# Performance work log

Measured on AMD Instinct MI355X. Metric: run time of the kernel, lower is better.

## Reference

```python
import math
import jax, jax.numpy as jnp
import numpy as np

N, T, F, H = 30000, 4, 128, 8  # num_node, num_type, num_fea, num_head
D = F // H


def setup_inputs() -> dict:
    key = jax.random.key(0)
    k0, k1, k2, k3, k4 = jax.random.split(key, 5)
    feature = jax.random.normal(k0, (N, F), dtype=jnp.float32)
    edge_fea = jax.random.normal(k1, (N, T, F), dtype=jnp.float32)
    node_multi_mask = jax.random.randint(k2, (N,), 0, T)
    # Xavier-uniform-like scale for [*, F, F] projection tables
    xav = math.sqrt(6.0 / (F + F))
    node_proj = jax.random.uniform(k3, (T, F, F), minval=-xav, maxval=xav, dtype=jnp.float32)
    edge_proj = jax.random.uniform(k4, (T * T, F, F), minval=-xav, maxval=xav, dtype=jnp.float32)
    return {
        "feature": feature,
        "edge_fea": edge_fea,
        "node_multi_mask": node_multi_mask,
        "node_proj": node_proj,
        "edge_proj": edge_proj,
    }


def reference(feature, edge_fea, node_multi_mask, node_proj, edge_proj):
    # Type-indexed projections. Instead of gathering per-node [F,F] matrices
    # (which would materialize N*F*F), compute projections for all T source
    # types in one batched einsum, then select each node's type with a gather.
    # node: out[n] = node_proj[mask[n]] @ feature[n]
    node_all = jnp.einsum('tgf,nf->ntg', node_proj, feature)           # [N,T,F]
    node_p = jnp.take_along_axis(node_all, node_multi_mask[:, None, None], axis=1)[:, 0]  # [N,F]
    # edge: out[n,j] = edge_proj[mask[n]*T + j] @ edge_fea[n,j]
    edge_proj_r = edge_proj.reshape(T, T, F, F)                         # [src_type, j, F, F]
    edge_all = jnp.einsum('stgf,ntf->nstg', edge_proj_r, edge_fea)      # [N,T_src,T,F]
    edge_p = jnp.take_along_axis(edge_all, node_multi_mask[:, None, None, None], axis=1)[:, 0]  # [N,T,F]

    # multi-head attention weights
    node_multi_in = node_p.reshape(N, 1, H, D).transpose(0, 2, 1, 3) / math.sqrt(D)  # [N,H,1,D]
    edge_multi_in = edge_p.reshape(N, T, H, D).transpose(0, 2, 3, 1)                  # [N,H,D,T]
    scores = jnp.matmul(node_multi_in, edge_multi_in)                                 # [N,H,1,T]
    # NOTE: original uses nn.Softmax(dim=1) -> softmax over the HEAD axis
    all_r_weight = jax.nn.softmax(scores, axis=1).transpose(0, 3, 1, 2)               # [N,T,H,1]
    return all_r_weight
```

## Files before the change

### kernel.cpp

```cpp
#include <hip/hip_runtime.h>
#include <hip/hip_bf16.h>

#define N_NODES 30000
#define T_TYPES 4
#define F_DIM   128
#define H_HEADS 8

typedef __bf16 bf16x8 __attribute__((ext_vector_type(8)));
typedef __bf16 bf16x4 __attribute__((ext_vector_type(4)));
typedef float  floatx4 __attribute__((ext_vector_type(4)));

#define WS_REORDER 64
#define WS_NPB     480256
#define WS_EPB     611328

template <int CTRL>
static __device__ __forceinline__ float dpp_add(float x) {
    int xi = __builtin_bit_cast(int, x);
    int yi = __builtin_amdgcn_update_dpp(xi, xi, CTRL, 0xF, 0xF, true);
    return x + __builtin_bit_cast(float, yi);
}
static __device__ __forceinline__ float sum16(float x) {
    x = dpp_add<0xB1>(x);
    x = dpp_add<0x4E>(x);
    x = dpp_add<0x141>(x);
    x = dpp_add<0x140>(x);
    return x;
}

__global__ __launch_bounds__(256) void prep_kernel(
    const float* __restrict__ node_proj, const float* __restrict__ edge_proj,
    __bf16* __restrict__ npb, __bf16* __restrict__ epb, int* __restrict__ counts)
{
    int i = blockIdx.x * 256 + threadIdx.x;
    if (i < 4) counts[i] = 0;
    int base = i * 4;
    float4 v;
    __bf16* dst;
    if (base < T_TYPES * F_DIM * F_DIM) {
        v = ((const float4*)node_proj)[i];
        dst = npb + base;
    } else {
        int off = base - T_TYPES * F_DIM * F_DIM;
        v = ((const float4*)edge_proj)[off >> 2];
        dst = epb + off;
    }
    bf16x4 w = { (__bf16)v.x, (__bf16)v.y, (__bf16)v.z, (__bf16)v.w };
    *(bf16x4*)dst = w;
}

__global__ __launch_bounds__(256) void bucket_kernel(
    const int* __restrict__ mask, int* __restrict__ counts, int* __restrict__ reorder)
{
    int n = blockIdx.x * 256 + threadIdx.x;
    int lane = threadIdx.x & 63;
    int t = (n < N_NODES) ? mask[n] : -1;
    #pragma unroll
    for (int tt = 0; tt < T_TYPES; ++tt) {
        unsigned long long b = __ballot(t == tt);
        if (b == 0ull) continue;
        int cnt = __popcll(b);
        int leader = __ffsll((unsigned long long)b) - 1;
        int base = 0;
        if (lane == leader) base = atomicAdd(&counts[tt], cnt);
        base = __shfl(base, leader);
        if (t == tt) {
            int prefix = __popcll(b & ((1ull << lane) - 1ull));
            reorder[tt * N_NODES + base + prefix] = n;
        }
    }
}

__global__ __launch_bounds__(512) void main_kernel(
    const float* __restrict__ feature, const float* __restrict__ edge_fea,
    const int* __restrict__ counts, const int* __restrict__ reorder,
    const __bf16* __restrict__ npb, const __bf16* __restrict__ epb,
    float* __restrict__ out)
{
    const int b = blockIdx.x;
    const int t = b & 3;
    const int start = (b >> 2) * 32;
    const int Nt = counts[t];
    if (start >= Nt) return;
    const int valid = min(32, Nt - start);

    __shared__ __bf16 Afeat[32][136];
    __shared__ __bf16 Aedge[4][32][136];
    __shared__ float  sc[32][4][H_HEADS];
    __shared__ int    nidx[32];

    const int tid = threadIdx.x;
    if (tid < 32) {
        int s = (tid < valid) ? tid : (valid - 1);
        nidx[tid] = reorder[t * N_NODES + start + s];
    }
    __syncthreads();

    const int colv = tid & 31;
    const int rowg = tid >> 5;
    #pragma unroll
    for (int it = 0; it < 2; ++it) {
        int row = it * 16 + rowg;
        float4 v = ((const float4*)(feature + (long)nidx[row] * F_DIM))[colv];
        bf16x4 w = { (__bf16)v.x, (__bf16)v.y, (__bf16)v.z, (__bf16)v.w };
        *(bf16x4*)(&Afeat[row][0] + colv * 4) = w;
    }
    #pragma unroll
    for (int it = 0; it < 8; ++it) {
        int row = it * 16 + rowg;
        int j = row >> 5, r = row & 31;
        float4 v = ((const float4*)(edge_fea + ((long)nidx[r] * 4 + j) * F_DIM))[colv];
        bf16x4 w = { (__bf16)v.x, (__bf16)v.y, (__bf16)v.z, (__bf16)v.w };
        *(bf16x4*)(&Aedge[j][r][0] + colv * 4) = w;
    }
    __syncthreads();

    const int lane = tid & 63;
    const int wave = tid >> 6;
    const int ml   = lane & 15;
    const int quad = lane >> 4;
    const int g0   = wave * 16;

    floatx4 accN[2] = {};
    {
        const __bf16* a0 = &Afeat[ml][quad * 8];
        const __bf16* a1 = &Afeat[16 + ml][quad * 8];
        const __bf16* b0 = npb + t * (F_DIM * F_DIM) + (g0 + ml) * F_DIM + quad * 8;
        #pragma unroll
        for (int k0 = 0; k0 < 128; k0 += 32) {
            bf16x8 A0 = *(const bf16x8*)(a0 + k0);
            bf16x8 A1 = *(const bf16x8*)(a1 + k0);
            bf16x8 B0 = *(const bf16x8*)(b0 + k0);
            accN[0] = __builtin_amdgcn_mfma_f32_16x16x32_bf16(A0, B0, accN[0], 0, 0, 0);
            accN[1] = __builtin_amdgcn_mfma_f32_16x16x32_bf16(A1, B0, accN[1], 0, 0, 0);
        }
    }

    #pragma unroll
    for (int j = 0; j < 4; ++j) {
        floatx4 accE[2] = {};
        const __bf16* a0 = &Aedge[j][ml][quad * 8];
        const __bf16* a1 = &Aedge[j][16 + ml][quad * 8];
        const __bf16* b0 = epb + (t * 4 + j) * (F_DIM * F_DIM) + (g0 + ml) * F_DIM + quad * 8;
        #pragma unroll
        for (int k0 = 0; k0 < 128; k0 += 32) {
            bf16x8 A0 = *(const bf16x8*)(a0 + k0);
            bf16x8 A1 = *(const bf16x8*)(a1 + k0);
            bf16x8 B0 = *(const bf16x8*)(b0 + k0);
            accE[0] = __builtin_amdgcn_mfma_f32_16x16x32_bf16(A0, B0, accE[0], 0, 0, 0);
            accE[1] = __builtin_amdgcn_mfma_f32_16x16x32_bf16(A1, B0, accE[1], 0, 0, 0);
        }
        #pragma unroll
        for (int mt = 0; mt < 2; ++mt) {
            floatx4 p = accN[mt] * accE[mt];
            p.x = sum16(p.x);
            p.y = sum16(p.y);
            p.z = sum16(p.z);
            p.w = sum16(p.w);
            if (ml == 0) {
                int mb = mt * 16 + quad * 4;
                sc[mb + 0][j][wave] = p.x * 0.25f;
                sc[mb + 1][j][wave] = p.y * 0.25f;
                sc[mb + 2][j][wave] = p.z * 0.25f;
                sc[mb + 3][j][wave] = p.w * 0.25f;
            }
        }
    }
    __syncthreads();

    if (tid < 128) {
        int node = tid >> 2, j = tid & 3;
        if (node < valid) {
            float v[8], m = -1e30f;
            #pragma unroll
            for (int h = 0; h < 8; ++h) { v[h] = sc[node][j][h]; m = fmaxf(m, v[h]); }
            float s = 0.f;
            #pragma unroll
            for (int h = 0; h < 8; ++h) { v[h] = __expf(v[h] - m); s += v[h]; }
            float r = 1.0f / s;
            float* o = out + (long)nidx[node] * (T_TYPES * H_HEADS) + j * H_HEADS;
            float4 o0 = { v[0] * r, v[1] * r, v[2] * r, v[3] * r };
            float4 o1 = { v[4] * r, v[5] * r, v[6] * r, v[7] * r };
            ((float4*)o)[0] = o0;
            ((float4*)o)[1] = o1;
        }
    }
}

extern "C" void kernel_launch(void* const* d_in, const int* in_sizes, int n_in,
                              void* d_out, int out_size, void* d_ws, size_t ws_size,
                              hipStream_t stream) {
    const float* feature   = (const float*)d_in[0];
    const float* edge_fea  = (const float*)d_in[1];
    const int*   mask      = (const int*)d_in[2];
    const float* node_proj = (const float*)d_in[3];
    const float* edge_proj = (const float*)d_in[4];
    float* out = (float*)d_out;

    char* ws = (char*)d_ws;
    int*    counts  = (int*)ws;
    int*    reorder = (int*)(ws + WS_REORDER);
    __bf16* npb     = (__bf16*)(ws + WS_NPB);
    __bf16* epb     = (__bf16*)(ws + WS_EPB);

    prep_kernel<<<320, 256, 0, stream>>>(node_proj, edge_proj, npb, epb, counts);
    bucket_kernel<<<(N_NODES + 255) / 256, 256, 0, stream>>>(mask, counts, reorder);
    int nblk = ((N_NODES + 31) / 32) * T_TYPES;
    main_kernel<<<nblk, 512, 0, stream>>>(feature, edge_fea, counts, reorder, npb, epb, out);
}
```

Baseline: 145.3 us.

## Replace type bucketing with dense all-type projection and masked score selection

Removes the bucket/reorder kernel and the per-type block grid. Each block now processes 32 consecutive nodes and computes projections for all four source types, keeping only the scores matching each node's type. This trades 4x more MFMA work for contiguous loads, one fewer launch, no atomics and no early-exiting blocks. Launch bounds also request higher occupancy.

New measurement: 196.0 us. 34.9% more time.

```diff
diff --git a/kernel.cpp b/kernel.cpp
--- a/kernel.cpp
+++ b/kernel.cpp
@@ -10,9 +10,8 @@
 typedef __bf16 bf16x4 __attribute__((ext_vector_type(4)));
 typedef float  floatx4 __attribute__((ext_vector_type(4)));
 
-#define WS_REORDER 64
-#define WS_NPB     480256
-#define WS_EPB     611328
+#define WS_NPB 0
+#define WS_EPB 131072
 
 template <int CTRL>
 static __device__ __forceinline__ float dpp_add(float x) {
@@ -30,10 +29,9 @@
 
 __global__ __launch_bounds__(256) void prep_kernel(
     const float* __restrict__ node_proj, const float* __restrict__ edge_proj,
-    __bf16* __restrict__ npb, __bf16* __restrict__ epb, int* __restrict__ counts)
+    __bf16* __restrict__ npb, __bf16* __restrict__ epb)
 {
     int i = blockIdx.x * 256 + threadIdx.x;
-    if (i < 4) counts[i] = 0;
     int base = i * 4;
     float4 v;
     __bf16* dst;
@@ -49,69 +47,42 @@
     *(bf16x4*)dst = w;
 }
 
-__global__ __launch_bounds__(256) void bucket_kernel(
-    const int* __restrict__ mask, int* __restrict__ counts, int* __restrict__ reorder)
-{
-    int n = blockIdx.x * 256 + threadIdx.x;
-    int lane = threadIdx.x & 63;
-    int t = (n < N_NODES) ? mask[n] : -1;
-    #pragma unroll
-    for (int tt = 0; tt < T_TYPES; ++tt) {
-        unsigned long long b = __ballot(t == tt);
-        if (b == 0ull) continue;
-        int cnt = __popcll(b);
-        int leader = __ffsll((unsigned long long)b) - 1;
-        int base = 0;
-        if (lane == leader) base = atomicAdd(&counts[tt], cnt);
-        base = __shfl(base, leader);
-        if (t == tt) {
-            int prefix = __popcll(b & ((1ull << lane) - 1ull));
-            reorder[tt * N_NODES + base + prefix] = n;
-        }
-    }
-}
-
-__global__ __launch_bounds__(512) void main_kernel(
+__global__ __launch_bounds__(512, 6) void main_kernel(
     const float* __restrict__ feature, const float* __restrict__ edge_fea,
-    const int* __restrict__ counts, const int* __restrict__ reorder,
+    const int* __restrict__ mask,
     const __bf16* __restrict__ npb, const __bf16* __restrict__ epb,
     float* __restrict__ out)
 {
     const int b = blockIdx.x;
-    const int t = b & 3;
-    const int start = (b >> 2) * 32;
-    const int Nt = counts[t];
-    if (start >= Nt) return;
-    const int valid = min(32, Nt - start);
+    const int n0 = b * 32;
+    const int valid = min(32, N_NODES - n0);
 
     __shared__ __bf16 Afeat[32][136];
     __shared__ __bf16 Aedge[4][32][136];
     __shared__ float  sc[32][4][H_HEADS];
-    __shared__ int    nidx[32];
+    __shared__ int    tys[32];
 
     const int tid = threadIdx.x;
-    if (tid < 32) {
-        int s = (tid < valid) ? tid : (valid - 1);
-        nidx[tid] = reorder[t * N_NODES + start + s];
-    }
-    __syncthreads();
+    if (tid < 32) tys[tid] = (tid < valid) ? mask[n0 + tid] : -1;
 
     const int colv = tid & 31;
     const int rowg = tid >> 5;
     #pragma unroll
     for (int it = 0; it < 2; ++it) {
         int row = it * 16 + rowg;
-        float4 v = ((const float4*)(feature + (long)nidx[row] * F_DIM))[colv];
+        int r = min(row, valid - 1);
+        float4 v = ((const float4*)(feature + (long)(n0 + r) * F_DIM))[colv];
         bf16x4 w = { (__bf16)v.x, (__bf16)v.y, (__bf16)v.z, (__bf16)v.w };
         *(bf16x4*)(&Afeat[row][0] + colv * 4) = w;
     }
     #pragma unroll
     for (int it = 0; it < 8; ++it) {
         int row = it * 16 + rowg;
-        int j = row >> 5, r = row & 31;
-        float4 v = ((const float4*)(edge_fea + ((long)nidx[r] * 4 + j) * F_DIM))[colv];
+        int j = row >> 5, r0 = row & 31;
+        int r = min(r0, valid - 1);
+        float4 v = ((const float4*)(edge_fea + ((long)(n0 + r) * 4 + j) * F_DIM))[colv];
         bf16x4 w = { (__bf16)v.x, (__bf16)v.y, (__bf16)v.z, (__bf16)v.w };
-        *(bf16x4*)(&Aedge[j][r][0] + colv * 4) = w;
+        *(bf16x4*)(&Aedge[j][r0][0] + colv * 4) = w;
     }
     __syncthreads();
 
@@ -121,48 +92,58 @@
     const int quad = lane >> 4;
     const int g0   = wave * 16;
 
-    floatx4 accN[2] = {};
-    {
-        const __bf16* a0 = &Afeat[ml][quad * 8];
-        const __bf16* a1 = &Afeat[16 + ml][quad * 8];
-        const __bf16* b0 = npb + t * (F_DIM * F_DIM) + (g0 + ml) * F_DIM + quad * 8;
-        #pragma unroll
-        for (int k0 = 0; k0 < 128; k0 += 32) {
-            bf16x8 A0 = *(const bf16x8*)(a0 + k0);
-            bf16x8 A1 = *(const bf16x8*)(a1 + k0);
-            bf16x8 B0 = *(const bf16x8*)(b0 + k0);
-            accN[0] = __builtin_amdgcn_mfma_f32_16x16x32_bf16(A0, B0, accN[0], 0, 0, 0);
-            accN[1] = __builtin_amdgcn_mfma_f32_16x16x32_bf16(A1, B0, accN[1], 0, 0, 0);
-        }
-    }
-
     #pragma unroll
-    for (int j = 0; j < 4; ++j) {
-        floatx4 accE[2] = {};
-        const __bf16* a0 = &Aedge[j][ml][quad * 8];
-        const __bf16* a1 = &Aedge[j][16 + ml][quad * 8];
-        const __bf16* b0 = epb + (t * 4 + j) * (F_DIM * F_DIM) + (g0 + ml) * F_DIM + quad * 8;
-        #pragma unroll
-        for (int k0 = 0; k0 < 128; k0 += 32) {
-            bf16x8 A0 = *(const bf16x8*)(a0 + k0);
-            bf16x8 A1 = *(const bf16x8*)(a1 + k0);
-            bf16x8 B0 = *(const bf16x8*)(b0 + k0);
-            accE[0] = __builtin_amdgcn_mfma_f32_16x16x32_bf16(A0, B0, accE[0], 0, 0, 0);
-            accE[1] = __builtin_amdgcn_mfma_f32_16x16x32_bf16(A1, B0, accE[1], 0, 0, 0);
+    for (int tg = 0; tg < 2; ++tg) {
+        floatx4 accN[2][2] = {};
+        {
+            const __bf16* a0 = &Afeat[ml][quad * 8];
+            const __bf16* a1 = &Afeat[16 + ml][quad * 8];
+            const __bf16* bp = npb + (tg * 2) * (F_DIM * F_DIM) + (g0 + ml) * F_DIM + quad * 8;
+            #pragma unroll
+            for (int k0 = 0; k0 < 128; k0 += 32) {
+                bf16x8 A0 = *(const bf16x8*)(a0 + k0);
+                bf16x8 A1 = *(const bf16x8*)(a1 + k0);
+                bf16x8 B0 = *(const bf16x8*)(bp + k0);
+                bf16x8 B1 = *(const bf16x8*)(bp + F_DIM * F_DIM + k0);
+                accN[0][0] = __builtin_amdgcn_mfma_f32_16x16x32_bf16(A0, B0, accN[0][0], 0, 0, 0);
+                accN[0][1] = __builtin_amdgcn_mfma_f32_16x16x32_bf16(A1, B0, accN[0][1], 0, 0, 0);
+                accN[1][0] = __builtin_amdgcn_mfma_f32_16x16x32_bf16(A0, B1, accN[1][0], 0, 0, 0);
+                accN[1][1] = __builtin_amdgcn_mfma_f32_16x16x32_bf16(A1, B1, accN[1][1], 0, 0, 0);
+            }
         }
         #pragma unroll
-        for (int mt = 0; mt < 2; ++mt) {
-            floatx4 p = accN[mt] * accE[mt];
-            p.x = sum16(p.x);
-            p.y = sum16(p.y);
-            p.z = sum16(p.z);
-            p.w = sum16(p.w);
-            if (ml == 0) {
-                int mb = mt * 16 + quad * 4;
-                sc[mb + 0][j][wave] = p.x * 0.25f;
-                sc[mb + 1][j][wave] = p.y * 0.25f;
-                sc[mb + 2][j][wave] = p.z * 0.25f;
-                sc[mb + 3][j][wave] = p.w * 0.25f;
+        for (int j = 0; j < 4; ++j) {
+            const __bf16* a0 = &Aedge[j][ml][quad * 8];
+            const __bf16* a1 = &Aedge[j][16 + ml][quad * 8];
+            #pragma unroll
+            for (int ti = 0; ti < 2; ++ti) {
+                const int t = tg * 2 + ti;
+                floatx4 accE0 = {0.f, 0.f, 0.f, 0.f};
+                floatx4 accE1 = {0.f, 0.f, 0.f, 0.f};
+                const __bf16* bp = epb + (t * 4 + j) * (F_DIM * F_DIM) + (g0 + ml) * F_DIM + quad * 8;
+                #pragma unroll
+                for (int k0 = 0; k0 < 128; k0 += 32) {
+                    bf16x8 A0 = *(const bf16x8*)(a0 + k0);
+                    bf16x8 A1 = *(const bf16x8*)(a1 + k0);
+                    bf16x8 B0 = *(const bf16x8*)(bp + k0);
+                    accE0 = __builtin_amdgcn_mfma_f32_16x16x32_bf16(A0, B0, accE0, 0, 0, 0);
+                    accE1 = __builtin_amdgcn_mfma_f32_16x16x32_bf16(A1, B0, accE1, 0, 0, 0);
+                }
+                #pragma unroll
+                for (int mt = 0; mt < 2; ++mt) {
+                    floatx4 p = accN[ti][mt] * (mt ? accE1 : accE0);
+                    p.x = sum16(p.x);
+                    p.y = sum16(p.y);
+                    p.z = sum16(p.z);
+                    p.w = sum16(p.w);
+                    if (ml == 0) {
+                        int mb = mt * 16 + quad * 4;
+                        if (tys[mb + 0] == t) sc[mb + 0][j][wave] = p.x * 0.25f;
+                        if (tys[mb + 1] == t) sc[mb + 1][j][wave] = p.y * 0.25f;
+                        if (tys[mb + 2] == t) sc[mb + 2][j][wave] = p.z * 0.25f;
+                        if (tys[mb + 3] == t) sc[mb + 3][j][wave] = p.w * 0.25f;
+                    }
+                }
             }
         }
     }
@@ -178,7 +159,7 @@
             #pragma unroll
             for (int h = 0; h < 8; ++h) { v[h] = __expf(v[h] - m); s += v[h]; }
             float r = 1.0f / s;
-            float* o = out + (long)nidx[node] * (T_TYPES * H_HEADS) + j * H_HEADS;
+            float* o = out + (long)(n0 + node) * (T_TYPES * H_HEADS) + j * H_HEADS;
             float4 o0 = { v[0] * r, v[1] * r, v[2] * r, v[3] * r };
             float4 o1 = { v[4] * r, v[5] * r, v[6] * r, v[7] * r };
             ((float4*)o)[0] = o0;
@@ -198,13 +179,10 @@
     float* out = (float*)d_out;
 
     char* ws = (char*)d_ws;
-    int*    counts  = (int*)ws;
-    int*    reorder = (int*)(ws + WS_REORDER);
-    __bf16* npb     = (__bf16*)(ws + WS_NPB);
-    __bf16* epb     = (__bf16*)(ws + WS_EPB);
+    __bf16* npb = (__bf16*)(ws + WS_NPB);
+    __bf16* epb = (__bf16*)(ws + WS_EPB);
 
-    prep_kernel<<<320, 256, 0, stream>>>(node_proj, edge_proj, npb, epb, counts);
-    bucket_kernel<<<(N_NODES + 255) / 256, 256, 0, stream>>>(mask, counts, reorder);
-    int nblk = ((N_NODES + 31) / 32) * T_TYPES;
-    main_kernel<<<nblk, 512, 0, stream>>>(feature, edge_fea, counts, reorder, npb, epb, out);
+    prep_kernel<<<320, 256, 0, stream>>>(node_proj, edge_proj, npb, epb);
+    int nblk = (N_NODES + 31) / 32;
+    main_kernel<<<nblk, 512, 0, stream>>>(feature, edge_fea, mask, npb, epb, out);
 }
```
